# Kernel tuning notes

Measured on AMD Instinct MI355X. Metric: run time of the kernel, lower is better.

## Reference

```python
import jax, jax.numpy as jnp
import numpy as np


def setup_inputs() -> dict:
    key = jax.random.key(0)
    ks = jax.random.split(key, 10)
    B, S, C, H, NC, T = 128, 512, 512, 512, 64, 25
    s = 0.02  # init scale
    return {
        "x": jax.random.normal(ks[0], (B, S, C), jnp.float32),
        "text": jax.random.randint(ks[1], (B, T + 1), 0, NC),
        "W_i2h": jax.random.normal(ks[2], (C, H), jnp.float32) * s,
        "W_h2h": jax.random.normal(ks[3], (H, H), jnp.float32) * s,
        "b_h2h": jnp.zeros((H,), jnp.float32),
        "W_score": jax.random.normal(ks[4], (H, 1), jnp.float32) * s,
        "W_lstm": jax.random.normal(ks[5], (C + NC, 4 * H), jnp.float32) * s,
        "U_lstm": jax.random.normal(ks[6], (H, 4 * H), jnp.float32) * s,
        "b_lstm": jnp.zeros((4 * H,), jnp.float32),
        "W_gen": jax.random.normal(ks[7], (H, NC), jnp.float32) * s,
        "b_gen": jnp.zeros((NC,), jnp.float32),
        "batch_max_length": 25,
    }


def reference(x, text, W_i2h, W_h2h, b_h2h, W_score, W_lstm, U_lstm, b_lstm,
              W_gen, b_gen, batch_max_length):
    B = x.shape[0]
    H = W_h2h.shape[0]
    NC = W_gen.shape[1]
    T = batch_max_length

    # i2h(batch_H) is loop-invariant -> compute once. [B,S,H]
    batch_H_proj = jnp.einsum('bsc,ch->bsh', x, W_i2h)
    # one-hot teacher-forcing inputs, time-major for scan. [T,B,NC]
    onehots_t = jnp.swapaxes(jax.nn.one_hot(text[:, :T], NC, dtype=x.dtype), 0, 1)

    def step(carry, char_oh):
        h, c = carry
        hp = (h @ W_h2h + b_h2h)[:, None, :]                 # [B,1,H]
        e = jnp.tanh(batch_H_proj + hp) @ W_score            # [B,S,1]
        alpha = jax.nn.softmax(e, axis=1)                    # [B,S,1]
        context = jnp.einsum('bs,bsc->bc', alpha[..., 0], x) # [B,C]
        inp = jnp.concatenate([context, char_oh], axis=1)    # [B,C+NC]
        # Keras LSTMCell gate math: z split into i,f,g,o chunks
        z = inp @ W_lstm + h @ U_lstm + b_lstm               # [B,4H]
        zi, zf, zg, zo = jnp.split(z, 4, axis=1)
        i = jax.nn.sigmoid(zi)
        f = jax.nn.sigmoid(zf)
        g = jnp.tanh(zg)
        o = jax.nn.sigmoid(zo)
        c_new = f * c + i * g
        h_new = o * jnp.tanh(c_new)
        return (h_new, c_new), h_new

    init = (jnp.zeros((B, H), x.dtype), jnp.zeros((B, H), x.dtype))
    _, hs = jax.lax.scan(step, init, onehots_t)              # [T,B,H]
    output_hiddens = jnp.swapaxes(hs, 0, 1)                  # [B,T,H]
    probs = output_hiddens @ W_gen + b_gen                   # [B,T,NC]
    return probs
```

## Files before the change

kernel.cpp:

```cpp
#include <hip/hip_runtime.h>
#include <hip/hip_bf16.h>

#define B_ 128
#define S_ 512
#define C_ 512
#define H_ 512
#define NC_ 64
#define T_ 25
#define TEXTW (T_ + 1)

typedef __attribute__((ext_vector_type(8))) short bf16x8;
typedef __attribute__((ext_vector_type(8))) unsigned short u16x8;
typedef __attribute__((ext_vector_type(4))) float f32x4;

__device__ __forceinline__ float bf2f(unsigned short u) {
    union { unsigned int i; float f; } v; v.i = ((unsigned int)u) << 16; return v.f;
}
__device__ __forceinline__ unsigned short f2bf(float f) {
    union { float f; unsigned int u; } v; v.f = f;
    unsigned int r = (v.u + 0x7FFFu + ((v.u >> 16) & 1u)) >> 16;
    return (unsigned short)r;
}
__device__ __forceinline__ void gload_lds16(const void* g, void* l) {
    __builtin_amdgcn_global_load_lds(
        (const __attribute__((address_space(1))) unsigned int*)g,
        (__attribute__((address_space(3))) unsigned int*)l, 16, 0, 0);
}
__device__ __forceinline__ float fast_tanh(float x) {
    float e = __builtin_amdgcn_exp2f(2.885390082f * x);
    return 1.f - 2.f * __builtin_amdgcn_rcpf(e + 1.f);
}
__device__ __forceinline__ float fast_sigmoid(float x) {
    return __builtin_amdgcn_rcpf(1.f + __builtin_amdgcn_exp2f(-1.442695041f * x));
}

__global__ __launch_bounds__(512) void setup_k(
    const float* __restrict__ Wi, const float* __restrict__ Wh,
    const float* __restrict__ Wl, const float* __restrict__ Ul,
    unsigned short* __restrict__ Wt_bf, unsigned short* __restrict__ Wh_bf,
    unsigned short* __restrict__ WU_t,
    float* __restrict__ c, unsigned short* __restrict__ inp) {
    int blk = blockIdx.x, tid = threadIdx.x;
    if (blk < 128) {
        c[blk * 512 + tid] = 0.f;
        inp[blk * 1024 + 512 + tid] = 0;
    } else if (blk < 640) {
        int n = blk - 128;
        Wt_bf[n * 512 + tid] = f2bf(Wi[tid * 512 + n]);
    } else if (blk < 1152) {
        int i = (blk - 640) * 512 + tid;
        Wh_bf[i] = f2bf(Wh[i]);
    } else {
        int np = blk - 1152;
        int h = np >> 2, g = np & 3;
        {
            float v = Wl[(size_t)tid * 2048 + g * 512 + h];
            WU_t[(size_t)np * 1024 + tid] = f2bf(v);
        }
        {
            float v = Ul[(size_t)tid * 2048 + g * 512 + h];
            WU_t[(size_t)np * 1024 + 512 + tid] = f2bf(v);
        }
    }
}

__global__ __launch_bounds__(256) void conv_x(const float* __restrict__ in,
                                              unsigned short* __restrict__ out) {
    int i = blockIdx.x * 256 + threadIdx.x;
    const float4 v = ((const float4*)in)[i];
    ushort4 o;
    o.x = f2bf(v.x); o.y = f2bf(v.y); o.z = f2bf(v.z); o.w = f2bf(v.w);
    ((ushort4*)out)[i] = o;
}

__global__ __launch_bounds__(256) void gemm_proj(const unsigned short* __restrict__ A,
                                                 const unsigned short* __restrict__ Bt,
                                                 unsigned short* __restrict__ Cm) {
    __shared__ unsigned short As[128 * 64];
    __shared__ unsigned short Bs[128 * 64];
    int tid = threadIdx.x;
    int lane = tid & 63;
    int wid = tid >> 6;
    int wr = wid >> 1, wc = wid & 1;
    int row0 = blockIdx.y * 128;
    int col0 = blockIdx.x * 128;

    f32x4 acc[4][4];
#pragma unroll
    for (int i = 0; i < 4; ++i)
#pragma unroll
        for (int j = 0; j < 4; ++j) acc[i][j] = (f32x4){0.f, 0.f, 0.f, 0.f};

    for (int k0 = 0; k0 < 512; k0 += 64) {
#pragma unroll
        for (int i = 0; i < 4; ++i) {
            int e = tid + i * 256;
            int r = e >> 3, cc = e & 7;
            int cs = cc ^ (r & 7);
            gload_lds16(A + (size_t)(row0 + r) * 512 + k0 + cs * 8, &As[e * 8]);
        }
#pragma unroll
        for (int i = 0; i < 4; ++i) {
            int e = tid + i * 256;
            int r = e >> 3, cc = e & 7;
            int cs = cc ^ (r & 7);
            gload_lds16(Bt + (size_t)(col0 + r) * 512 + k0 + cs * 8, &Bs[e * 8]);
        }
        __syncthreads();
#pragma unroll
        for (int ks = 0; ks < 2; ++ks) {
            bf16x8 a[4], b[4];
#pragma unroll
            for (int i = 0; i < 4; ++i) {
                int m = wr * 64 + i * 16 + (lane & 15);
                int ch = (ks * 4 + (lane >> 4)) ^ (m & 7);
                a[i] = *(const bf16x8*)&As[(m * 8 + ch) * 8];
            }
#pragma unroll
            for (int j = 0; j < 4; ++j) {
                int n = wc * 64 + j * 16 + (lane & 15);
                int ch = (ks * 4 + (lane >> 4)) ^ (n & 7);
                b[j] = *(const bf16x8*)&Bs[(n * 8 + ch) * 8];
            }
#pragma unroll
            for (int i = 0; i < 4; ++i)
#pragma unroll
                for (int j = 0; j < 4; ++j)
                    acc[i][j] = __builtin_amdgcn_mfma_f32_16x16x32_bf16(a[i], b[j], acc[i][j], 0, 0, 0);
        }
        __syncthreads();
    }
#pragma unroll
    for (int i = 0; i < 4; ++i)
#pragma unroll
        for (int j = 0; j < 4; ++j) {
            int gcol = col0 + wc * 64 + j * 16 + (lane & 15);
#pragma unroll
            for (int r = 0; r < 4; ++r) {
                int grow = row0 + wr * 64 + i * 16 + (lane >> 4) * 4 + r;
                Cm[(size_t)grow * 512 + gcol] = f2bf(acc[i][j][r]);
            }
        }
}

__global__ __launch_bounds__(512) void z_gemm(const unsigned short* __restrict__ A,
                                              const unsigned short* __restrict__ Bt,
                                              float* __restrict__ Z) {
    __shared__ unsigned short As[8192];
    __shared__ unsigned short Bs[4096];
    int tid = threadIdx.x;
    int lane = tid & 63;
    int wave = tid >> 6;
    int wr = wave >> 2, wc = wave & 3;
    int col0 = blockIdx.x * 64;

    f32x4 acc[4];
#pragma unroll
    for (int i = 0; i < 4; ++i) acc[i] = (f32x4){0.f, 0.f, 0.f, 0.f};

    for (int k0 = 0; k0 < 1024; k0 += 64) {
#pragma unroll
        for (int i = 0; i < 2; ++i) {
            int e = tid + i * 512;
            int r = e >> 3, cc = e & 7;
            int cs = cc ^ (r & 7);
            gload_lds16(A + (size_t)r * 1024 + k0 + cs * 8, &As[e * 8]);
        }
        {
            int e = tid;
            int r = e >> 3, cc = e & 7;
            int cs = cc ^ (r & 7);
            gload_lds16(Bt + (size_t)(col0 + r) * 1024 + k0 + cs * 8, &Bs[e * 8]);
        }
        __syncthreads();
#pragma unroll
        for (int ks = 0; ks < 2; ++ks) {
            bf16x8 a[4], bfr;
#pragma unroll
            for (int i = 0; i < 4; ++i) {
                int m = wr * 64 + i * 16 + (lane & 15);
                int ch = (ks * 4 + (lane >> 4)) ^ (m & 7);
                a[i] = *(const bf16x8*)&As[(m * 8 + ch) * 8];
            }
            {
                int n = wc * 16 + (lane & 15);
                int ch = (ks * 4 + (lane >> 4)) ^ (n & 7);
                bfr = *(const bf16x8*)&Bs[(n * 8 + ch) * 8];
            }
#pragma unroll
            for (int i = 0; i < 4; ++i)
                acc[i] = __builtin_amdgcn_mfma_f32_16x16x32_bf16(a[i], bfr, acc[i], 0, 0, 0);
        }
        __syncthreads();
    }
#pragma unroll
    for (int i = 0; i < 4; ++i) {
        int gcol = col0 + wc * 16 + (lane & 15);
#pragma unroll
        for (int r = 0; r < 4; ++r) {
            int grow = wr * 64 + i * 16 + (lane >> 4) * 4 + r;
            Z[(size_t)grow * 2048 + gcol] = acc[i][r];
        }
    }
}

__global__ __launch_bounds__(1024) void ghp_ectx(
    const float* __restrict__ z, const int* __restrict__ text,
    const float* __restrict__ Wl, const float* __restrict__ bl,
    const unsigned short* __restrict__ Whb, const float* __restrict__ bh2h,
    float* __restrict__ c, float* __restrict__ hs_t,
    unsigned short* __restrict__ inp,
    const unsigned short* __restrict__ proj, const unsigned short* __restrict__ xb,
    const float* __restrict__ Wscore, int t) {
    __shared__ float shg[512];
    __shared__ float gp[16][512];
    __shared__ float sh_hp[512];
    __shared__ float sh_e[512];
    __shared__ float sh_alpha[512];
    __shared__ float sh_red[16];
    __shared__ float shp[8][512];
    int b = blockIdx.x;
    int tid = threadIdx.x, wave = tid >> 6, lane = tid & 63;

    if (t >= 0) {
        if (tid < 512) {
            int ch = text[b * TEXTW + t];
            const float* wrow = Wl + (size_t)(512 + ch) * 2048;
            float4 zv = *(const float4*)(z + (size_t)b * 2048 + tid * 4);
            float zi = zv.x + bl[tid] + wrow[tid];
            float zf = zv.y + bl[512 + tid] + wrow[512 + tid];
            float zg = zv.z + bl[1024 + tid] + wrow[1024 + tid];
            float zo = zv.w + bl[1536 + tid] + wrow[1536 + tid];
            float ig = fast_sigmoid(zi);
            float fg = fast_sigmoid(zf);
            float gg = fast_tanh(zg);
            float og = fast_sigmoid(zo);
            int idx = b * 512 + tid;
            float cn = fg * c[idx] + ig * gg;
            c[idx] = cn;
            float hn = og * fast_tanh(cn);
            hs_t[idx] = hn;
            inp[b * 1024 + 512 + tid] = f2bf(hn);
            shg[tid] = hn;
        }
        __syncthreads();
        if (t >= T_ - 1) return;
        {
            float r8[8] = {0.f, 0.f, 0.f, 0.f, 0.f, 0.f, 0.f, 0.f};
#pragma unroll 4
            for (int kk = 0; kk < 32; ++kk) {
                int k = wave * 32 + kk;
                float hv = shg[k];
                u16x8 wv = *(const u16x8*)(Whb + k * 512 + lane * 8);
#pragma unroll
                for (int jj = 0; jj < 8; ++jj) r8[jj] = fmaf(hv, bf2f(wv[jj]), r8[jj]);
            }
#pragma unroll
            for (int jj = 0; jj < 8; ++jj) gp[wave][lane * 8 + jj] = r8[jj];
        }
        __syncthreads();
        if (tid < 512) {
            float s = bh2h[tid];
#pragma unroll
            for (int w = 0; w < 16; ++w) s += gp[w][tid];
            sh_hp[tid] = s;
        }
        __syncthreads();
    } else {
        if (tid < 512) sh_hp[tid] = bh2h[tid];
        __syncthreads();
    }

    {
        float4 h0 = *(const float4*)(sh_hp + lane * 8);
        float4 h1 = *(const float4*)(sh_hp + lane * 8 + 4);
        float4 w0 = *(const float4*)(Wscore + lane * 8);
        float4 w1 = *(const float4*)(Wscore + lane * 8 + 4);
        float hp_r[8] = {h0.x, h0.y, h0.z, h0.w, h1.x, h1.y, h1.z, h1.w};
        float w_r[8]  = {w0.x, w0.y, w0.z, w0.w, w1.x, w1.y, w1.z, w1.w};
        float w2_r[8];
#pragma unroll
        for (int j = 0; j < 8; ++j) w2_r[j] = -2.f * w_r[j];
        int s0 = wave * 32;
        for (int i = 0; i < 32; i += 4) {
            bf16x8 pv[4];
#pragma unroll
            for (int q = 0; q < 4; ++q)
                pv[q] = *(const bf16x8*)(proj + ((size_t)(b * 512 + s0 + i + q) << 9) + lane * 8);
#pragma unroll
            for (int q = 0; q < 4; ++q) {
                float a = 0.f;
#pragma unroll
                for (int j = 0; j < 8; ++j) {
                    float xv = bf2f((unsigned short)pv[q][j]) + hp_r[j];
                    float r = __builtin_amdgcn_rcpf(__builtin_amdgcn_exp2f(2.885390082f * xv) + 1.f);
                    a += w_r[j];
                    a = fmaf(w2_r[j], r, a);
                }
#pragma unroll
                for (int off = 32; off > 0; off >>= 1) a += __shfl_xor(a, off, 64);
                if (lane == 0) sh_e[s0 + i + q] = a;
            }
        }
    }
    __syncthreads();

    if (tid < 512) {
        float v = sh_e[tid];
        float m = v;
#pragma unroll
        for (int off = 32; off > 0; off >>= 1) m = fmaxf(m, __shfl_xor(m, off, 64));
        if (lane == 0) sh_red[wave] = m;
    }
    __syncthreads();
    if (tid < 512) {
        float v = sh_e[tid];
        float mm = sh_red[0];
#pragma unroll
        for (int i = 1; i < 8; ++i) mm = fmaxf(mm, sh_red[i]);
        float p = __builtin_amdgcn_exp2f(1.442695041f * (v - mm));
        float ss = p;
#pragma unroll
        for (int off = 32; off > 0; off >>= 1) ss += __shfl_xor(ss, off, 64);
        if (lane == 0) sh_red[8 + wave] = ss;
        sh_alpha[tid] = p;
    }
    __syncthreads();
    {
        float tot = 0.f;
#pragma unroll
        for (int i = 0; i < 8; ++i) tot += sh_red[8 + i];
        float inv = __builtin_amdgcn_rcpf(tot);
        inv = inv * (2.f - tot * inv);
        if (tid < 512) sh_alpha[tid] = sh_alpha[tid] * inv;
    }
    __syncthreads();

    {
        int cc = wave >> 3, sg = wave & 7;
        int col = cc * 256 + lane * 4;
        float a0 = 0.f, a1 = 0.f, a2 = 0.f, a3 = 0.f;
#pragma unroll 4
        for (int s = sg; s < 512; s += 8) {
            float al = sh_alpha[s];
            ushort4 xv = *(const ushort4*)(xb + ((size_t)(b * 512 + s) << 9) + col);
            a0 = fmaf(al, bf2f(xv.x), a0);
            a1 = fmaf(al, bf2f(xv.y), a1);
            a2 = fmaf(al, bf2f(xv.z), a2);
            a3 = fmaf(al, bf2f(xv.w), a3);
        }
        *(float4*)&shp[sg][col] = make_float4(a0, a1, a2, a3);
    }
    __syncthreads();
    if (tid < 512) {
        float s = 0.f;
#pragma unroll
        for (int r = 0; r < 8; ++r) s += shp[r][tid];
        inp[b * 1024 + tid] = f2bf(s);
    }
}

__global__ __launch_bounds__(64) void gen_probs(const float* __restrict__ hs,
                                                const float* __restrict__ Wg,
                                                const float* __restrict__ bg,
                                                float* __restrict__ out) {
    __shared__ float sh[512];
    int bt = blockIdx.x;
    int b = bt / T_, t = bt % T_;
    int tid = threadIdx.x;
    const float* hrow = hs + ((size_t)t * B_ + b) * H_;
    for (int i = tid; i < 512; i += 64) sh[i] = hrow[i];
    __syncthreads();
    float acc = bg[tid];
#pragma unroll 4
    for (int k = 0; k < 512; ++k) acc = fmaf(sh[k], Wg[k * 64 + tid], acc);
    out[(size_t)bt * 64 + tid] = acc;
}

extern "C" void kernel_launch(void* const* d_in, const int* in_sizes, int n_in,
                              void* d_out, int out_size, void* d_ws, size_t ws_size,
                              hipStream_t stream) {
    const float* x       = (const float*)d_in[0];
    const int*   text    = (const int*)d_in[1];
    const float* W_i2h   = (const float*)d_in[2];
    const float* W_h2h   = (const float*)d_in[3];
    const float* b_h2h   = (const float*)d_in[4];
    const float* W_score = (const float*)d_in[5];
    const float* W_lstm  = (const float*)d_in[6];
    const float* U_lstm  = (const float*)d_in[7];
    const float* b_lstm  = (const float*)d_in[8];
    const float* W_gen   = (const float*)d_in[9];
    const float* b_gen   = (const float*)d_in[10];
    float* out = (float*)d_out;

    char* ws = (char*)d_ws;
    unsigned short* x_bf    = (unsigned short*)ws;
    unsigned short* proj_bf = (unsigned short*)(ws + 67108864);
    unsigned short* Wt_bf   = (unsigned short*)(ws + 134217728);
    unsigned short* Wh_bf   = (unsigned short*)(ws + 134742016);
    unsigned short* WU_t    = (unsigned short*)(ws + 135266304);
    float* c_buf   = (float*)(ws + 139460608);
    unsigned short* inp_bf = (unsigned short*)(ws + 140247040);
    float* z_buf   = (float*)(ws + 140509184);
    float* hs      = (float*)(ws + 141557760);

    setup_k<<<dim3(3200), 512, 0, stream>>>(W_i2h, W_h2h, W_lstm, U_lstm,
                                            Wt_bf, Wh_bf, WU_t, c_buf, inp_bf);
    conv_x<<<dim3(32768), 256, 0, stream>>>(x, x_bf);
    gemm_proj<<<dim3(4, 512), 256, 0, stream>>>(x_bf, Wt_bf, proj_bf);
    ghp_ectx<<<dim3(128), 1024, 0, stream>>>(z_buf, text, W_lstm, b_lstm, Wh_bf, b_h2h,
                                             c_buf, hs, inp_bf, proj_bf, x_bf, W_score, -1);
    for (int t = 0; t < T_; ++t) {
        z_gemm<<<dim3(32), 512, 0, stream>>>(inp_bf, WU_t, z_buf);
        ghp_ectx<<<dim3(128), 1024, 0, stream>>>(z_buf, text, W_lstm, b_lstm, Wh_bf, b_h2h,
                                                 c_buf, hs + (size_t)t * (B_ * H_),
                                                 inp_bf, proj_bf, x_bf, W_score, t);
    }
    gen_probs<<<dim3(B_ * T_), 64, 0, stream>>>(hs, W_gen, b_gen, out);
}
```

Measured before the change: 1.494 ms.

## Split attention over sequence halves with flash-style softmax merge in z_gemm

The per-step attention kernel now runs 256 blocks, each handling half of the sequence for one batch row. Each block writes an unnormalized partial context plus its local max and sum. The z_gemm A-tile load merges the two halves with log-sum-exp weights and converts to bf16. This doubles occupancy on the latency-bound recurrent step. The cost is that both halves redundantly recompute the LSTM cell and the h2h projection, and the merge adds extra fp32 traffic.

```diff
diff --git a/kernel.cpp b/kernel.cpp
--- a/kernel.cpp
+++ b/kernel.cpp
@@ -39,10 +39,11 @@
     const float* __restrict__ Wl, const float* __restrict__ Ul,
     unsigned short* __restrict__ Wt_bf, unsigned short* __restrict__ Wh_bf,
     unsigned short* __restrict__ WU_t,
-    float* __restrict__ c, unsigned short* __restrict__ inp) {
+    float* __restrict__ c2, unsigned short* __restrict__ inp) {
     int blk = blockIdx.x, tid = threadIdx.x;
     if (blk < 128) {
-        c[blk * 512 + tid] = 0.f;
+        c2[blk * 512 + tid] = 0.f;
+        c2[65536 + blk * 512 + tid] = 0.f;
         inp[blk * 1024 + 512 + tid] = 0;
     } else if (blk < 640) {
         int n = blk - 128;
@@ -143,9 +144,10 @@
         }
 }
 
-__global__ __launch_bounds__(512) void z_gemm(const unsigned short* __restrict__ A,
-                                              const unsigned short* __restrict__ Bt,
-                                              float* __restrict__ Z) {
+__global__ __launch_bounds__(512) void z_gemm(
+    const unsigned short* __restrict__ inp, const unsigned short* __restrict__ Bt,
+    const float* __restrict__ pc, const float* __restrict__ pm,
+    const float* __restrict__ ps, float* __restrict__ Z) {
     __shared__ unsigned short As[8192];
     __shared__ unsigned short Bs[4096];
     int tid = threadIdx.x;
@@ -154,17 +156,55 @@
     int wr = wave >> 2, wc = wave & 3;
     int col0 = blockIdx.x * 64;
 
+    float cw0[2], cw1[2];
+    int rr[2], csv[2];
+#pragma unroll
+    for (int i = 0; i < 2; ++i) {
+        int e = tid + i * 512;
+        int r = e >> 3, cc = e & 7;
+        rr[i] = r; csv[i] = cc ^ (r & 7);
+        float m0 = pm[r], m1 = pm[128 + r];
+        float s0 = ps[r], s1 = ps[128 + r];
+        float M = fmaxf(m0, m1);
+        float w0 = __builtin_amdgcn_exp2f(1.442695041f * (m0 - M));
+        float w1 = __builtin_amdgcn_exp2f(1.442695041f * (m1 - M));
+        float inv = 1.f / (w0 * s0 + w1 * s1);
+        cw0[i] = w0 * inv; cw1[i] = w1 * inv;
+    }
+
     f32x4 acc[4];
 #pragma unroll
     for (int i = 0; i < 4; ++i) acc[i] = (f32x4){0.f, 0.f, 0.f, 0.f};
 
     for (int k0 = 0; k0 < 1024; k0 += 64) {
-#pragma unroll
-        for (int i = 0; i < 2; ++i) {
-            int e = tid + i * 512;
-            int r = e >> 3, cc = e & 7;
-            int cs = cc ^ (r & 7);
-            gload_lds16(A + (size_t)r * 1024 + k0 + cs * 8, &As[e * 8]);
+        if (k0 < 512) {
+#pragma unroll
+            for (int i = 0; i < 2; ++i) {
+                int e = tid + i * 512;
+                int kb = k0 + csv[i] * 8;
+                const float* c0p = pc + rr[i] * 512 + kb;
+                const float* c1p = pc + 65536 + rr[i] * 512 + kb;
+                float4 c0a = *(const float4*)c0p;
+                float4 c0b = *(const float4*)(c0p + 4);
+                float4 c1a = *(const float4*)c1p;
+                float4 c1b = *(const float4*)(c1p + 4);
+                u16x8 o;
+                o[0] = f2bf(cw0[i] * c0a.x + cw1[i] * c1a.x);
+                o[1] = f2bf(cw0[i] * c0a.y + cw1[i] * c1a.y);
+                o[2] = f2bf(cw0[i] * c0a.z + cw1[i] * c1a.z);
+                o[3] = f2bf(cw0[i] * c0a.w + cw1[i] * c1a.w);
+                o[4] = f2bf(cw0[i] * c0b.x + cw1[i] * c1b.x);
+                o[5] = f2bf(cw0[i] * c0b.y + cw1[i] * c1b.y);
+                o[6] = f2bf(cw0[i] * c0b.z + cw1[i] * c1b.z);
+                o[7] = f2bf(cw0[i] * c0b.w + cw1[i] * c1b.w);
+                *(u16x8*)&As[e * 8] = o;
+            }
+        } else {
+#pragma unroll
+            for (int i = 0; i < 2; ++i) {
+                int e = tid + i * 512;
+                gload_lds16(inp + (size_t)rr[i] * 1024 + k0 + csv[i] * 8, &As[e * 8]);
+            }
         }
         {
             int e = tid;
@@ -204,22 +244,24 @@
     }
 }
 
-__global__ __launch_bounds__(1024) void ghp_ectx(
+__global__ __launch_bounds__(1024) void ghp_e2(
     const float* __restrict__ z, const int* __restrict__ text,
     const float* __restrict__ Wl, const float* __restrict__ bl,
     const unsigned short* __restrict__ Whb, const float* __restrict__ bh2h,
-    float* __restrict__ c, float* __restrict__ hs_t,
+    float* __restrict__ c2, float* __restrict__ hs_t,
     unsigned short* __restrict__ inp,
     const unsigned short* __restrict__ proj, const unsigned short* __restrict__ xb,
-    const float* __restrict__ Wscore, int t) {
+    const float* __restrict__ Wscore,
+    float* __restrict__ pc, float* __restrict__ pm, float* __restrict__ ps, int t) {
     __shared__ float shg[512];
     __shared__ float gp[16][512];
     __shared__ float sh_hp[512];
-    __shared__ float sh_e[512];
-    __shared__ float sh_alpha[512];
-    __shared__ float sh_red[16];
+    __shared__ float sh_e[256];
+    __shared__ float sh_alpha[256];
+    __shared__ float sh_red[8];
     __shared__ float shp[8][512];
-    int b = blockIdx.x;
+    int blk = blockIdx.x;
+    int half = blk >> 7, b = blk & 127;
     int tid = threadIdx.x, wave = tid >> 6, lane = tid & 63;
 
     if (t >= 0) {
@@ -235,12 +277,14 @@
             float fg = fast_sigmoid(zf);
             float gg = fast_tanh(zg);
             float og = fast_sigmoid(zo);
-            int idx = b * 512 + tid;
-            float cn = fg * c[idx] + ig * gg;
-            c[idx] = cn;
+            int idx = half * 65536 + b * 512 + tid;
+            float cn = fg * c2[idx] + ig * gg;
+            c2[idx] = cn;
             float hn = og * fast_tanh(cn);
-            hs_t[idx] = hn;
-            inp[b * 1024 + 512 + tid] = f2bf(hn);
+            if (half == 0) {
+                hs_t[b * 512 + tid] = hn;
+                inp[b * 1024 + 512 + tid] = f2bf(hn);
+            }
             shg[tid] = hn;
         }
         __syncthreads();
@@ -281,12 +325,12 @@
         float w2_r[8];
 #pragma unroll
         for (int j = 0; j < 8; ++j) w2_r[j] = -2.f * w_r[j];
-        int s0 = wave * 32;
-        for (int i = 0; i < 32; i += 4) {
+        int s0g = half * 256 + wave * 16;
+        for (int i = 0; i < 16; i += 4) {
             bf16x8 pv[4];
 #pragma unroll
             for (int q = 0; q < 4; ++q)
-                pv[q] = *(const bf16x8*)(proj + ((size_t)(b * 512 + s0 + i + q) << 9) + lane * 8);
+                pv[q] = *(const bf16x8*)(proj + ((size_t)(b * 512 + s0g + i + q) << 9) + lane * 8);
 #pragma unroll
             for (int q = 0; q < 4; ++q) {
                 float a = 0.f;
@@ -299,13 +343,13 @@
                 }
 #pragma unroll
                 for (int off = 32; off > 0; off >>= 1) a += __shfl_xor(a, off, 64);
-                if (lane == 0) sh_e[s0 + i + q] = a;
+                if (lane == 0) sh_e[wave * 16 + i + q] = a;
             }
         }
     }
     __syncthreads();
 
-    if (tid < 512) {
+    if (tid < 256) {
         float v = sh_e[tid];
         float m = v;
 #pragma unroll
@@ -313,36 +357,29 @@
         if (lane == 0) sh_red[wave] = m;
     }
     __syncthreads();
-    if (tid < 512) {
-        float v = sh_e[tid];
-        float mm = sh_red[0];
-#pragma unroll
-        for (int i = 1; i < 8; ++i) mm = fmaxf(mm, sh_red[i]);
-        float p = __builtin_amdgcn_exp2f(1.442695041f * (v - mm));
+    if (tid < 256) {
+        float mh = fmaxf(fmaxf(sh_red[0], sh_red[1]), fmaxf(sh_red[2], sh_red[3]));
+        float p = __builtin_amdgcn_exp2f(1.442695041f * (sh_e[tid] - mh));
         float ss = p;
 #pragma unroll
         for (int off = 32; off > 0; off >>= 1) ss += __shfl_xor(ss, off, 64);
-        if (lane == 0) sh_red[8 + wave] = ss;
+        if (lane == 0) sh_red[4 + wave] = ss;
         sh_alpha[tid] = p;
     }
     __syncthreads();
-    {
-        float tot = 0.f;
-#pragma unroll
-        for (int i = 0; i < 8; ++i) tot += sh_red[8 + i];
-        float inv = __builtin_amdgcn_rcpf(tot);
-        inv = inv * (2.f - tot * inv);
-        if (tid < 512) sh_alpha[tid] = sh_alpha[tid] * inv;
-    }
-    __syncthreads();
+    if (tid == 0) {
+        pm[half * 128 + b] = fmaxf(fmaxf(sh_red[0], sh_red[1]), fmaxf(sh_red[2], sh_red[3]));
+        ps[half * 128 + b] = sh_red[4] + sh_red[5] + sh_red[6] + sh_red[7];
+    }
 
     {
         int cc = wave >> 3, sg = wave & 7;
         int col = cc * 256 + lane * 4;
         float a0 = 0.f, a1 = 0.f, a2 = 0.f, a3 = 0.f;
 #pragma unroll 4
-        for (int s = sg; s < 512; s += 8) {
-            float al = sh_alpha[s];
+        for (int sl = sg; sl < 256; sl += 8) {
+            float al = sh_alpha[sl];
+            int s = half * 256 + sl;
             ushort4 xv = *(const ushort4*)(xb + ((size_t)(b * 512 + s) << 9) + col);
             a0 = fmaf(al, bf2f(xv.x), a0);
             a1 = fmaf(al, bf2f(xv.y), a1);
@@ -356,7 +393,7 @@
         float s = 0.f;
 #pragma unroll
         for (int r = 0; r < 8; ++r) s += shp[r][tid];
-        inp[b * 1024 + tid] = f2bf(s);
+        pc[(size_t)(half * 128 + b) * 512 + tid] = s;
     }
 }
 
@@ -399,22 +436,27 @@
     unsigned short* Wt_bf   = (unsigned short*)(ws + 134217728);
     unsigned short* Wh_bf   = (unsigned short*)(ws + 134742016);
     unsigned short* WU_t    = (unsigned short*)(ws + 135266304);
-    float* c_buf   = (float*)(ws + 139460608);
-    unsigned short* inp_bf = (unsigned short*)(ws + 140247040);
-    float* z_buf   = (float*)(ws + 140509184);
-    float* hs      = (float*)(ws + 141557760);
+    float* c2      = (float*)(ws + 139460608);
+    unsigned short* inp_bf = (unsigned short*)(ws + 139984896);
+    float* z_buf   = (float*)(ws + 140247040);
+    float* pc      = (float*)(ws + 141295616);
+    float* pm      = (float*)(ws + 141819904);
+    float* ps      = (float*)(ws + 141820928);
+    float* hs      = (float*)(ws + 141821952);
 
     setup_k<<<dim3(3200), 512, 0, stream>>>(W_i2h, W_h2h, W_lstm, U_lstm,
-                                            Wt_bf, Wh_bf, WU_t, c_buf, inp_bf);
+                                            Wt_bf, Wh_bf, WU_t, c2, inp_bf);
     conv_x<<<dim3(32768), 256, 0, stream>>>(x, x_bf);
     gemm_proj<<<dim3(4, 512), 256, 0, stream>>>(x_bf, Wt_bf, proj_bf);
-    ghp_ectx<<<dim3(128), 1024, 0, stream>>>(z_buf, text, W_lstm, b_lstm, Wh_bf, b_h2h,
-                                             c_buf, hs, inp_bf, proj_bf, x_bf, W_score, -1);
+    ghp_e2<<<dim3(256), 1024, 0, stream>>>(z_buf, text, W_lstm, b_lstm, Wh_bf, b_h2h,
+                                           c2, hs, inp_bf, proj_bf, x_bf, W_score,
+                                           pc, pm, ps, -1);
     for (int t = 0; t < T_; ++t) {
-        z_gemm<<<dim3(32), 512, 0, stream>>>(inp_bf, WU_t, z_buf);
-        ghp_ectx<<<dim3(128), 1024, 0, stream>>>(z_buf, text, W_lstm, b_lstm, Wh_bf, b_h2h,
-                                                 c_buf, hs + (size_t)t * (B_ * H_),
-                                                 inp_bf, proj_bf, x_bf, W_score, t);
+        z_gemm<<<dim3(32), 512, 0, stream>>>(inp_bf, WU_t, pc, pm, ps, z_buf);
+        ghp_e2<<<dim3(256), 1024, 0, stream>>>(z_buf, text, W_lstm, b_lstm, Wh_bf, b_h2h,
+                                               c2, hs + (size_t)t * (B_ * H_),
+                                               inp_bf, proj_bf, x_bf, W_score,
+                                               pc, pm, ps, t);
     }
     gen_probs<<<dim3(B_ * T_), 64, 0, stream>>>(hs, W_gen, b_gen, out);
 }
```

Result: no change. 1.468 ms (-1.7%).
